# Performance work log

Measured on AMD Instinct MI355X. Metric: run time of the kernel, lower is better.

Reference implementation:

```python
import jax, jax.numpy as jnp
import numpy as np
import math

B = 64        # graphs per batch
NPG = 2048    # nodes per graph
DEG = 4       # avg degree
EPG = NPG * DEG
N = B * NPG
E = B * EPG
F_IN = 4
H = 128
K1 = math.ceil(0.8 * NPG)   # 1639
K2 = math.ceil(0.8 * K1)    # 1312
K3 = math.ceil(0.8 * K2)    # 1050
ACT = 124


def setup_inputs() -> dict:
    key = jax.random.key(0)
    ks = jax.random.split(key, 20)
    x = jax.random.normal(ks[0], (N, F_IN), jnp.float32)
    off = (jnp.arange(B, dtype=jnp.int32) * NPG)[:, None]
    src = (jax.random.randint(ks[1], (B, EPG), 0, NPG, jnp.int32) + off).reshape(-1)
    dst = (jax.random.randint(ks[2], (B, EPG), 0, NPG, jnp.int32) + off).reshape(-1)

    def lin(k, fi, fo):
        return (jax.random.normal(k, (fi, fo), jnp.float32) / np.sqrt(fi)).astype(jnp.float32)

    return dict(
        x=x, src=src, dst=dst,
        W1=lin(ks[3], F_IN, H), b1=jnp.zeros((H,), jnp.float32),
        W2=lin(ks[4], H, H),    b2=jnp.zeros((H,), jnp.float32),
        W3=lin(ks[5], H, H),    b3=jnp.zeros((H,), jnp.float32),
        p1=jax.random.normal(ks[6], (H,), jnp.float32),
        p2=jax.random.normal(ks[7], (H,), jnp.float32),
        p3=jax.random.normal(ks[8], (H,), jnp.float32),
        lw1=lin(ks[9], 2 * H, H),  lb1=jnp.zeros((H,), jnp.float32),
        lw2=lin(ks[10], H, 64),    lb2=jnp.zeros((64,), jnp.float32),
        lw3=lin(ks[11], 64, ACT),  lb3=jnp.zeros((ACT,), jnp.float32),
    )


def gcn(x, W, b, src, dst, emask, n_nodes):
    # PyG GCNConv: add self loops, sym-norm deg^-1/2 A deg^-1/2, then bias
    h = x @ W                                  # [n, H]
    w = emask.astype(x.dtype)                  # [E]
    deg = jax.ops.segment_sum(w, dst, num_segments=n_nodes) + 1.0  # +1 self loop
    dis = jax.lax.rsqrt(deg)
    coef = dis[src] * dis[dst] * w             # [E]
    out = jax.ops.segment_sum(h[src] * coef[:, None], dst, num_segments=n_nodes)
    out = out + h * (dis * dis)[:, None]       # self-loop contribution
    return out + b


def topk_pool(x, p, src, dst, emask, n_per_graph, k):
    # TopKPooling: score = tanh(x.p/||p||); keep top ceil(ratio*n) per graph;
    # x_out = x[perm] * score[perm]; drop edges not fully inside kept set.
    score = jnp.tanh((x @ p) / jnp.linalg.norm(p))       # [B*n]
    vals, idx = jax.lax.top_k(score.reshape(B, n_per_graph), k)  # [B,k]
    xg = x.reshape(B, n_per_graph, -1)
    x_new = (jnp.take_along_axis(xg, idx[:, :, None], axis=1) * vals[:, :, None])
    x_new = x_new.reshape(B * k, -1)
    flat_idx = (idx + (jnp.arange(B, dtype=jnp.int32) * n_per_graph)[:, None]).reshape(-1)
    new_pos = jnp.full((B * n_per_graph,), -1, jnp.int32)
    new_pos = new_pos.at[flat_idx].set(jnp.arange(B * k, dtype=jnp.int32))
    ns, nd = new_pos[src], new_pos[dst]
    valid = emask & (ns >= 0) & (nd >= 0)
    ns = jnp.where(valid, ns, 0)
    nd = jnp.where(valid, nd, 0)
    return x_new, ns, nd, valid


def readout(x, k):
    # global_max_pool || global_mean_pool (uniform graph sizes)
    xr = x.reshape(B, k, -1)
    return jnp.concatenate([xr.max(axis=1), xr.mean(axis=1)], axis=1)  # [B, 2H]


def reference(x, src, dst, W1, b1, W2, b2, W3, b3, p1, p2, p3,
              lw1, lb1, lw2, lb2, lw3, lb3):
    emask = jnp.ones((E,), bool)
    h = jax.nn.relu(gcn(x, W1, b1, src, dst, emask, N))
    h, s1, d1, m1 = topk_pool(h, p1, src, dst, emask, NPG, K1)
    x1 = readout(h, K1)
    h = jax.nn.relu(gcn(h, W2, b2, s1, d1, m1, B * K1))
    h, s2, d2, m2 = topk_pool(h, p2, s1, d1, m1, K1, K2)
    x2 = readout(h, K2)
    h = jax.nn.relu(gcn(h, W3, b3, s2, d2, m2, B * K2))
    h, s3, d3, m3 = topk_pool(h, p3, s2, d2, m2, K2, K3)
    x3 = readout(h, K3)
    z = x1 + x2 + x3                                # [B, 256]
    z = jax.nn.relu(z @ lw1 + lb1)
    z = jax.nn.relu(z @ lw2 + lb2)
    # F.dropout(p=0.5) is identity in eval mode
    out = jax.nn.sigmoid(z @ lw3 + lb3)             # [B, 124]; squeeze(1) is no-op
    return out
```

## Files before the change

### kernel.cpp

```cpp
#include <hip/hip_runtime.h>
#include <math.h>

namespace {
constexpr int B_   = 64;
constexpr int NPG  = 2048;
constexpr int N0   = B_ * NPG;
constexpr int E0   = N0 * 4;
constexpr int H_   = 128;
constexpr int K1   = 1639, K2 = 1312, K3 = 1050;
constexpr int N1   = B_ * K1;
constexpr int N2   = B_ * K2;
constexpr int N3   = B_ * K3;
constexpr int ACT  = 124;
constexpr int RS   = 32;
}

typedef short bf16x8 __attribute__((ext_vector_type(8)));
typedef float f32x4  __attribute__((ext_vector_type(4)));

__device__ __forceinline__ unsigned short f2bf(float f)
{
    unsigned x = __float_as_uint(f);
    x = x + 0x7FFFu + ((x >> 16) & 1u);
    return (unsigned short)(x >> 16);
}

__global__ void pack_k(const float* __restrict__ W, unsigned short* __restrict__ WT)
{
    int t = blockIdx.x * 256 + threadIdx.x;
    int n = t >> 7, k = t & 127;
    WT[n * 128 + k] = f2bf(W[k * 128 + n]);
}

__global__ __launch_bounds__(256) void mmh_k(const float* __restrict__ Xin,
                                             const int* __restrict__ selOld,
                                             const float* __restrict__ score,
                                             const unsigned short* __restrict__ WT,
                                             float* __restrict__ C, int M)
{
    __shared__ unsigned short sA[64 * 128];
    char* sAb = (char*)sA;
    int tid = threadIdx.x;
    int row0 = blockIdx.x * 64;
    #pragma unroll
    for (int ch = 0; ch < 8; ++ch) {
        int i = ch * 1024 + tid * 4;
        int r = i >> 7, c = i & 127;
        int g = selOld[row0 + r];
        float sc = score[g];
        float4 v = *(const float4*)(Xin + (size_t)g * H_ + c);
        unsigned short h0 = f2bf(v.x * sc), h1 = f2bf(v.y * sc);
        unsigned short h2 = f2bf(v.z * sc), h3 = f2bf(v.w * sc);
        unsigned int lo = (unsigned int)h0 | ((unsigned int)h1 << 16);
        unsigned int hi = (unsigned int)h2 | ((unsigned int)h3 << 16);
        int off = (r * 256 + c * 2) ^ ((r & 7) << 4);
        *(unsigned int*)(sAb + off)     = lo;
        *(unsigned int*)(sAb + off + 4) = hi;
    }
    __syncthreads();

    int w    = tid >> 6;
    int lane = tid & 63;
    int l16  = lane & 15;
    int lq   = lane >> 4;
    int arow = w * 16 + l16;
    int abase = (arow * 256) ^ ((arow & 7) << 4);

    f32x4 acc[8];
    #pragma unroll
    for (int ct = 0; ct < 8; ++ct) acc[ct] = (f32x4){0.f, 0.f, 0.f, 0.f};

    #pragma unroll
    for (int ks = 0; ks < 4; ++ks) {
        int aoff = (arow * 256 + ks * 64 + lq * 16) ^ ((arow & 7) << 4);
        bf16x8 af = *(const bf16x8*)(sAb + aoff);
        #pragma unroll
        for (int ct = 0; ct < 8; ++ct) {
            const unsigned short* bp = WT + (ct * 16 + l16) * 128 + ks * 32 + lq * 8;
            bf16x8 bf = *(const bf16x8*)bp;
            acc[ct] = __builtin_amdgcn_mfma_f32_16x16x32_bf16(af, bf, acc[ct], 0, 0, 0);
        }
    }
    #pragma unroll
    for (int ct = 0; ct < 8; ++ct) {
        int col = ct * 16 + l16;
        int rb  = row0 + w * 16 + lq * 4;
        C[(size_t)(rb + 0) * H_ + col] = acc[ct][0];
        C[(size_t)(rb + 1) * H_ + col] = acc[ct][1];
        C[(size_t)(rb + 2) * H_ + col] = acc[ct][2];
        C[(size_t)(rb + 3) * H_ + col] = acc[ct][3];
    }
}

__global__ void count_deg_k(const int* __restrict__ dst, int E, int* __restrict__ deg)
{
    int e = blockIdx.x * blockDim.x + threadIdx.x;
    if (e < E) atomicAdd(deg + dst[e], 1);
}

__global__ __launch_bounds__(1024) void scan1_k(const int* __restrict__ in, int* __restrict__ out,
                                                int* __restrict__ bsum, int n)
{
    __shared__ int s[1024];
    int t = threadIdx.x;
    int i = blockIdx.x * 1024 + t;
    int v = (i < n) ? in[i] : 0;
    s[t] = v;
    __syncthreads();
    for (int d = 1; d < 1024; d <<= 1) {
        int add = (t >= d) ? s[t - d] : 0;
        __syncthreads();
        s[t] += add;
        __syncthreads();
    }
    if (i < n) out[i] = s[t] - v;
    if (t == 1023) bsum[blockIdx.x] = s[1023];
}

__global__ __launch_bounds__(256) void scan2_k(int* __restrict__ bsum, int nb,
                                               int* __restrict__ totalOut,
                                               const float* __restrict__ p,
                                               float* __restrict__ invnOut)
{
    __shared__ int s[256];
    __shared__ float ps[128];
    int t = threadIdx.x;
    int v = (t < nb) ? bsum[t] : 0;
    s[t] = v;
    if (p && t < 128) ps[t] = p[t] * p[t];
    __syncthreads();
    for (int d = 1; d < 256; d <<= 1) {
        int add = (t >= d) ? s[t - d] : 0;
        __syncthreads();
        s[t] += add;
        __syncthreads();
    }
    if (t < nb) bsum[t] = s[t] - v;
    if (t == 0 && totalOut) *totalOut = s[255];
    for (int d = 64; d > 0; d >>= 1) {
        if (p && t < d) ps[t] += ps[t + d];
        __syncthreads();
    }
    if (p && t == 0) *invnOut = rsqrtf(ps[0]);
}

__global__ void scan3_k(int* __restrict__ out, const int* __restrict__ bsum, int n,
                        const int* __restrict__ deg, float* __restrict__ dis)
{
    int i = blockIdx.x * blockDim.x + threadIdx.x;
    if (i < n) {
        out[i] += bsum[i >> 10];
        dis[i] = rsqrtf((float)deg[i] + 1.0f);
    }
}

__global__ void fill_k(const int* __restrict__ src, const int* __restrict__ dst, int E,
                       const int* __restrict__ rowoff, int* __restrict__ cur,
                       int* __restrict__ esrc)
{
    int e = blockIdx.x * blockDim.x + threadIdx.x;
    if (e >= E) return;
    int d = dst[e];
    int pos = rowoff[d] + atomicAdd(cur + d, 1);
    esrc[pos] = src[e];
}

__global__ void remap_count_k(const int* __restrict__ osrc, const int* __restrict__ odst,
                              const int* __restrict__ ecntIn, int fixedE,
                              const int* __restrict__ newpos, int* __restrict__ deg)
{
    int E = ecntIn ? *ecntIn : fixedE;
    int e = blockIdx.x * blockDim.x + threadIdx.x;
    if (e >= E) return;
    int ns = newpos[osrc[e]];
    int nd = newpos[odst[e]];
    if (ns >= 0 && nd >= 0) atomicAdd(deg + nd, 1);
}

__global__ void remap_fill_k(const int* __restrict__ osrc, const int* __restrict__ odst,
                             const int* __restrict__ ecntIn, int fixedE,
                             const int* __restrict__ newpos, const int* __restrict__ rowoff,
                             int* __restrict__ cur,
                             int* __restrict__ esrc, int* __restrict__ edst)
{
    int E = ecntIn ? *ecntIn : fixedE;
    int e = blockIdx.x * blockDim.x + threadIdx.x;
    if (e >= E) return;
    int ns = newpos[osrc[e]];
    int nd = newpos[odst[e]];
    if (ns >= 0 && nd >= 0) {
        int pos = rowoff[nd] + atomicAdd(cur + nd, 1);
        esrc[pos] = ns;
        edst[pos] = nd;
    }
}

__global__ __launch_bounds__(256) void aggx_k(const float* __restrict__ X,
                                              const int* __restrict__ rowoff,
                                              const int* __restrict__ esrc,
                                              const float* __restrict__ dis,
                                              const float* __restrict__ W1,
                                              const float* __restrict__ b1,
                                              const float* __restrict__ p1,
                                              const float* __restrict__ invn,
                                              float* __restrict__ out,
                                              float* __restrict__ score,
                                              int npg, int Gb)
{
    __shared__ float sW[512];
    __shared__ float sb[128];
    __shared__ float sp[128];
    __shared__ float sxa[256 * 4];
    __shared__ float sdt[256];
    int tid = threadIdx.x;
    for (int i = tid; i < 512; i += 256) sW[i] = W1[i];
    if (tid < 128) { sb[tid] = b1[tid]; sp[tid] = p1[tid]; }
    int pb = blockIdx.x;
    int x8 = pb & 7;
    int m  = pb >> 3;
    int g  = x8 + 8 * (m / Gb);
    int lb = m % Gb;
    int nbase = g * npg + lb * 256;
    int n = nbase + tid;
    float dn = dis[n];
    float4 xa = *(const float4*)(X + (size_t)n * 4);
    float s2 = dn * dn;
    xa.x *= s2; xa.y *= s2; xa.z *= s2; xa.w *= s2;
    int beg = rowoff[n], end = rowoff[n + 1];
    for (int e = beg; e < end; ++e) {
        int s = esrc[e];
        float c = dis[s] * dn;
        float4 xs = *(const float4*)(X + (size_t)s * 4);
        xa.x += xs.x * c; xa.y += xs.y * c; xa.z += xs.z * c; xa.w += xs.w * c;
    }
    *(float4*)(sxa + tid * 4) = xa;
    __syncthreads();
    int wv = tid >> 6;
    int lane = tid & 63;
    int c0 = lane * 2;
    float wa0 = sW[c0],     wb0 = sW[128 + c0],     wc0 = sW[256 + c0],     wd0 = sW[384 + c0];
    float wa1 = sW[c0 + 1], wb1 = sW[128 + c0 + 1], wc1 = sW[256 + c0 + 1], wd1 = sW[384 + c0 + 1];
    float bb0 = sb[c0], bb1 = sb[c0 + 1];
    float pp0 = sp[c0], pp1 = sp[c0 + 1];
    #pragma unroll 4
    for (int ii = 0; ii < 64; ++ii) {
        int i = wv * 64 + ii;
        float4 a = *(const float4*)(sxa + i * 4);
        float o0 = fmaxf(a.x * wa0 + a.y * wb0 + a.z * wc0 + a.w * wd0 + bb0, 0.f);
        float o1 = fmaxf(a.x * wa1 + a.y * wb1 + a.z * wc1 + a.w * wd1 + bb1, 0.f);
        ((float2*)(out + (size_t)(nbase + i) * H_))[lane] = make_float2(o0, o1);
        float dt = o0 * pp0 + o1 * pp1;
        for (int mm = 32; mm > 0; mm >>= 1) dt += __shfl_xor(dt, mm);
        if (lane == 0) sdt[i] = dt;
    }
    __syncthreads();
    score[nbase + tid] = tanhf(sdt[tid] * invn[0]);
}

__global__ __launch_bounds__(256) void agg_k(const float* __restrict__ Hf,
                                             const int* __restrict__ rowoff,
                                             const int* __restrict__ esrc,
                                             const float* __restrict__ dis,
                                             const float* __restrict__ bias,
                                             const float* __restrict__ p,
                                             const float* __restrict__ invn,
                                             float* __restrict__ out,
                                             float* __restrict__ score,
                                             int npg, int Gb)
{
    int pb = blockIdx.x;
    int x8 = pb & 7;
    int m  = pb >> 3;
    int g  = x8 + 8 * (m / Gb);
    int lb = m % Gb;
    int j  = lb * 4 + (threadIdx.x >> 6);
    if (j >= npg) return;
    int n = g * npg + j;
    int lane = threadIdx.x & 63;
    int half = lane >> 5;
    int l4 = (lane & 31) * 4;
    float dn = dis[n];
    int beg = rowoff[n], end = rowoff[n + 1];
    float4 acc = make_float4(0.f, 0.f, 0.f, 0.f);
    for (int e = beg + half; e < end; e += 2) {
        int s = esrc[e];
        float c = dis[s] * dn;
        float4 v = *(const float4*)(Hf + (size_t)s * H_ + l4);
        acc.x += v.x * c; acc.y += v.y * c; acc.z += v.z * c; acc.w += v.w * c;
    }
    acc.x += __shfl_xor(acc.x, 32);
    acc.y += __shfl_xor(acc.y, 32);
    acc.z += __shfl_xor(acc.z, 32);
    acc.w += __shfl_xor(acc.w, 32);
    if (half == 0) {
        float4 hv = *(const float4*)(Hf + (size_t)n * H_ + l4);
        float4 bv = *(const float4*)(bias + l4);
        float s2 = dn * dn;
        float o0 = fmaxf(acc.x + hv.x * s2 + bv.x, 0.f);
        float o1 = fmaxf(acc.y + hv.y * s2 + bv.y, 0.f);
        float o2 = fmaxf(acc.z + hv.z * s2 + bv.z, 0.f);
        float o3 = fmaxf(acc.w + hv.w * s2 + bv.w, 0.f);
        *(float4*)(out + (size_t)n * H_ + l4) = make_float4(o0, o1, o2, o3);
        float4 pv = *(const float4*)(p + l4);
        float dt = o0 * pv.x + o1 * pv.y + o2 * pv.z + o3 * pv.w;
        for (int mm = 16; mm > 0; mm >>= 1) dt += __shfl_xor(dt, mm);
        if ((lane & 31) == 0) score[n] = tanhf(dt * invn[0]);
    }
}

__global__ __launch_bounds__(1024) void radix_topk_k(const float* __restrict__ score,
                                                     int n, int k,
                                                     int* __restrict__ selOld,
                                                     int* __restrict__ newpos)
{
    __shared__ unsigned long long key[2048];
    __shared__ int hist[256];
    __shared__ int sufs[256];
    __shared__ unsigned long long sh_prefix;
    __shared__ int sh_r, sh_done, sh_v, sh_rbin;
    __shared__ int cnt;
    int b = blockIdx.x;
    int t = threadIdx.x;
    const float* s = score + (size_t)b * n;
    #pragma unroll
    for (int h = 0; h < 2; ++h) {
        int i = t + h * 1024;
        unsigned long long pk = 0ull;
        if (i < n) {
            unsigned u = __float_as_uint(s[i]);
            u = (u & 0x80000000u) ? ~u : (u | 0x80000000u);
            pk = ((unsigned long long)u << 32) | (unsigned)(65535 - i);
        }
        key[i] = pk;
    }
    if (t == 0) { sh_prefix = 0ull; sh_r = k; sh_done = 0; cnt = 0; }
    __syncthreads();

    for (int lvl = 0; lvl < 8; ++lvl) {
        if (sh_done) break;
        int bs = 56 - 8 * lvl;
        if (t < 256) hist[t] = 0;
        __syncthreads();
        unsigned long long pref = sh_prefix;
        #pragma unroll
        for (int h = 0; h < 2; ++h) {
            int i = t + h * 1024;
            unsigned long long kk = key[i];
            if (kk != 0ull) {
                bool match = (lvl == 0) || ((kk >> (bs + 8)) == (pref >> (bs + 8)));
                if (match) atomicAdd(&hist[(int)((kk >> bs) & 255)], 1);
            }
        }
        __syncthreads();
        if (t < 256) sufs[t] = hist[t];
        __syncthreads();
        for (int d = 1; d < 256; d <<= 1) {
            int add = (t < 256 && t + d < 256) ? sufs[t + d] : 0;
            __syncthreads();
            if (t < 256) sufs[t] += add;
            __syncthreads();
        }
        if (t < 256) {
            int above = (t == 255) ? 0 : sufs[t + 1];
            if (sufs[t] >= sh_r && above < sh_r) {
                sh_v = t;
                sh_rbin = sh_r - above;
            }
        }
        __syncthreads();
        if (t == 0) {
            int v = sh_v;
            sh_prefix |= ((unsigned long long)v) << bs;
            sh_r = sh_rbin;
            if (hist[v] == sh_rbin) sh_done = 1;
        }
        __syncthreads();
    }
    unsigned long long thr = sh_prefix;
    #pragma unroll
    for (int h = 0; h < 2; ++h) {
        int i = t + h * 1024;
        if (i < n && key[i] >= thr) {
            int pos = atomicAdd(&cnt, 1);
            int oldg = b * n + i;
            selOld[b * k + pos] = oldg;
            newpos[oldg] = b * k + pos;
        }
    }
}

__global__ __launch_bounds__(512) void readout_part_k(const float* __restrict__ X,
                                                      const int* __restrict__ selOld,
                                                      const float* __restrict__ score,
                                                      int kRows, float* __restrict__ part)
{
    __shared__ float smax[16][128];
    __shared__ float ssum[16][128];
    int b = blockIdx.x / RS;
    int s = blockIdx.x % RS;
    int chunk = (kRows + RS - 1) / RS;
    int j0 = s * chunk;
    int j1 = min(kRows, j0 + chunk);
    int tid = threadIdx.x;
    int f4 = (tid & 31) * 4;
    int q = tid >> 5;
    float4 mx = make_float4(-3.4e38f, -3.4e38f, -3.4e38f, -3.4e38f);
    float4 sm = make_float4(0.f, 0.f, 0.f, 0.f);
    for (int j = j0 + q; j < j1; j += 16) {
        int g = selOld[b * kRows + j];
        float sc = score[g];
        float4 v = *(const float4*)(X + (size_t)g * H_ + f4);
        v.x *= sc; v.y *= sc; v.z *= sc; v.w *= sc;
        mx.x = fmaxf(mx.x, v.x); mx.y = fmaxf(mx.y, v.y);
        mx.z = fmaxf(mx.z, v.z); mx.w = fmaxf(mx.w, v.w);
        sm.x += v.x; sm.y += v.y; sm.z += v.z; sm.w += v.w;
    }
    *(float4*)&smax[q][f4] = mx;
    *(float4*)&ssum[q][f4] = sm;
    __syncthreads();
    if (tid < 128) {
        float m = smax[0][tid], a = ssum[0][tid];
        #pragma unroll
        for (int gq = 1; gq < 16; ++gq) {
            m = fmaxf(m, smax[gq][tid]);
            a += ssum[gq][tid];
        }
        float* pr = part + ((size_t)b * RS + s) * 256;
        pr[tid] = m;
        pr[128 + tid] = a;
    }
}

__global__ __launch_bounds__(256) void head_k(const float* __restrict__ part1,
                                              const float* __restrict__ part2,
                                              const float* __restrict__ part3,
                                              const float* __restrict__ lw1, const float* __restrict__ lb1,
                                              const float* __restrict__ lw2, const float* __restrict__ lb2,
                                              const float* __restrict__ lw3, const float* __restrict__ lb3,
                                              float* __restrict__ out)
{
    __shared__ float sZ[256];
    __shared__ float sZ1[128];
    __shared__ float sZ2[64];
    __shared__ float red[256];
    int b = blockIdx.x;
    int t = threadIdx.x;
    {
        int f = t & 127;
        const float* pr1 = part1 + (size_t)b * RS * 256;
        const float* pr2 = part2 + (size_t)b * RS * 256;
        const float* pr3 = part3 + (size_t)b * RS * 256;
        float zv;
        if (t < 128) {
            float m1 = -3.4e38f, m2 = -3.4e38f, m3 = -3.4e38f;
            #pragma unroll
            for (int s = 0; s < RS; ++s) {
                m1 = fmaxf(m1, pr1[s * 256 + f]);
                m2 = fmaxf(m2, pr2[s * 256 + f]);
                m3 = fmaxf(m3, pr3[s * 256 + f]);
            }
            zv = m1 + m2 + m3;
        } else {
            float s1 = 0.f, s2 = 0.f, s3 = 0.f;
            #pragma unroll
            for (int s = 0; s < RS; ++s) {
                s1 += pr1[s * 256 + 128 + f];
                s2 += pr2[s * 256 + 128 + f];
                s3 += pr3[s * 256 + 128 + f];
            }
            zv = s1 * (1.0f / (float)K1) + s2 * (1.0f / (float)K2) + s3 * (1.0f / (float)K3);
        }
        sZ[t] = zv;
    }
    __syncthreads();
    {
        int c = t & 127, h = t >> 7;
        float acc = 0.f;
        #pragma unroll
        for (int i = 0; i < 128; ++i) {
            int ii = h * 128 + i;
            acc += sZ[ii] * lw1[ii * 128 + c];
        }
        red[t] = acc;
        __syncthreads();
        if (t < 128) sZ1[t] = fmaxf(red[t] + red[128 + t] + lb1[t], 0.f);
        __syncthreads();
    }
    {
        int c = t & 63, q = t >> 6;
        float acc = 0.f;
        #pragma unroll
        for (int i = 0; i < 32; ++i) {
            int ii = q * 32 + i;
            acc += sZ1[ii] * lw2[ii * 64 + c];
        }
        red[t] = acc;
        __syncthreads();
        if (t < 64) sZ2[t] = fmaxf(red[t] + red[64 + t] + red[128 + t] + red[192 + t] + lb2[t], 0.f);
        __syncthreads();
    }
    {
        if (t < 2 * ACT) {
            int c = t >> 1, h = t & 1;
            float acc = 0.f;
            #pragma unroll
            for (int i = 0; i < 32; ++i) {
                int ii = h * 32 + i;
                acc += sZ2[ii] * lw3[ii * ACT + c];
            }
            red[t] = acc;
        }
        __syncthreads();
        if (t < ACT) {
            float s = red[2 * t] + red[2 * t + 1] + lb3[t];
            out[b * ACT + t] = 1.f / (1.f + expf(-s));
        }
    }
}

extern "C" void kernel_launch(void* const* d_in, const int* in_sizes, int n_in,
                              void* d_out, int out_size, void* d_ws, size_t ws_size,
                              hipStream_t stream)
{
    const float* x   = (const float*)d_in[0];
    const int*   src = (const int*)d_in[1];
    const int*   dst = (const int*)d_in[2];
    const float* W1  = (const float*)d_in[3];
    const float* b1  = (const float*)d_in[4];
    const float* W2  = (const float*)d_in[5];
    const float* b2  = (const float*)d_in[6];
    const float* W3  = (const float*)d_in[7];
    const float* b3  = (const float*)d_in[8];
    const float* p1  = (const float*)d_in[9];
    const float* p2  = (const float*)d_in[10];
    const float* p3  = (const float*)d_in[11];
    const float* lw1 = (const float*)d_in[12];
    const float* lb1 = (const float*)d_in[13];
    const float* lw2 = (const float*)d_in[14];
    const float* lb2 = (const float*)d_in[15];
    const float* lw3 = (const float*)d_in[16];
    const float* lb3 = (const float*)d_in[17];

    char* w = (char*)d_ws;
    size_t off = 0;
    auto alloc = [&](size_t bytes) -> void* {
        void* p = w + off;
        off = (off + bytes + 255) & ~(size_t)255;
        return p;
    };
    float* fA     = (float*)alloc((size_t)N0 * H_ * 4);
    float* fB     = (float*)alloc((size_t)N0 * H_ * 4);
    float* score  = (float*)alloc((size_t)N0 * 4);
    int*   newpos = (int*)  alloc((size_t)N0 * 4);
    int*   deg    = (int*)  alloc((size_t)(N0 + 1) * 4);
    int*   cur    = (int*)  alloc((size_t)N0 * 4);
    float* dis    = (float*)alloc((size_t)(N0 + 1) * 4);
    int*   selOld = (int*)  alloc((size_t)N1 * 4);
    int*   rowoff = (int*)  alloc((size_t)(N0 + 1) * 4);
    int*   bsum   = (int*)  alloc((size_t)1024 * 4);
    int*   cs0    = (int*)  alloc((size_t)E0 * 4);
    int*   cs1    = (int*)  alloc((size_t)E0 * 4);
    int*   cd1    = (int*)  alloc((size_t)E0 * 4);
    int*   cs2    = (int*)  alloc((size_t)E0 * 4);
    int*   cd2    = (int*)  alloc((size_t)E0 * 4);
    float* part1  = (float*)alloc((size_t)B_ * RS * 256 * 4);
    float* part2  = (float*)alloc((size_t)B_ * RS * 256 * 4);
    float* part3  = (float*)alloc((size_t)B_ * RS * 256 * 4);
    unsigned short* WT2 = (unsigned short*)alloc((size_t)128 * 128 * 2);
    unsigned short* WT3 = (unsigned short*)alloc((size_t)128 * 128 * 2);
    int*   ecnt   = (int*)  alloc(256);
    float* invn   = (float*)alloc(256);

    const size_t degcur_bytes = (size_t)((char*)cur - (char*)deg) + (size_t)N0 * 4;

    auto scan_rowoff = [&](int nNodes, int* totalOut, const float* p) {
        int n = nNodes + 1;
        int nb = (n + 1023) / 1024;
        scan1_k<<<nb, 1024, 0, stream>>>(deg, rowoff, bsum, n);
        scan2_k<<<1, 256, 0, stream>>>(bsum, nb, totalOut, p, invn);
        scan3_k<<<(n + 255) / 256, 256, 0, stream>>>(rowoff, bsum, n, deg, dis);
    };

    const int GbX = NPG / 256;
    const int Gb1 = (K1 + 3) / 4;
    const int Gb2 = (K2 + 3) / 4;

    pack_k<<<64, 256, 0, stream>>>(W2, WT2);
    pack_k<<<64, 256, 0, stream>>>(W3, WT3);

    hipMemsetAsync(deg, 0, degcur_bytes, stream);
    count_deg_k<<<E0 / 256, 256, 0, stream>>>(dst, E0, deg);
    scan_rowoff(N0, nullptr, p1);
    fill_k<<<E0 / 256, 256, 0, stream>>>(src, dst, E0, rowoff, cur, cs0);
    aggx_k<<<B_ * GbX, 256, 0, stream>>>(x, rowoff, cs0, dis, W1, b1, p1, invn, fB, score, NPG, GbX);

    hipMemsetAsync(newpos, 0xFF, (size_t)N0 * 4, stream);
    radix_topk_k<<<B_, 1024, 0, stream>>>(score, NPG, K1, selOld, newpos);
    readout_part_k<<<B_ * RS, 512, 0, stream>>>(fB, selOld, score, K1, part1);

    hipMemsetAsync(deg, 0, degcur_bytes, stream);
    remap_count_k<<<E0 / 256, 256, 0, stream>>>(src, dst, nullptr, E0, newpos, deg);
    scan_rowoff(N1, ecnt, p2);
    remap_fill_k<<<E0 / 256, 256, 0, stream>>>(src, dst, nullptr, E0, newpos, rowoff, cur, cs1, cd1);

    mmh_k<<<N1 / 64, 256, 0, stream>>>(fB, selOld, score, WT2, fA, N1);
    agg_k<<<B_ * Gb1, 256, 0, stream>>>(fA, rowoff, cs1, dis, b2, p2, invn, fB, score, K1, Gb1);

    hipMemsetAsync(newpos, 0xFF, (size_t)N1 * 4, stream);
    radix_topk_k<<<B_, 1024, 0, stream>>>(score, K1, K2, selOld, newpos);
    readout_part_k<<<B_ * RS, 512, 0, stream>>>(fB, selOld, score, K2, part2);

    hipMemsetAsync(deg, 0, degcur_bytes, stream);
    remap_count_k<<<E0 / 256, 256, 0, stream>>>(cs1, cd1, ecnt, 0, newpos, deg);
    scan_rowoff(N2, nullptr, p3);
    remap_fill_k<<<E0 / 256, 256, 0, stream>>>(cs1, cd1, ecnt, 0, newpos, rowoff, cur, cs2, cd2);

    mmh_k<<<N2 / 64, 256, 0, stream>>>(fB, selOld, score, WT3, fA, N2);
    agg_k<<<B_ * Gb2, 256, 0, stream>>>(fA, rowoff, cs2, dis, b3, p3, invn, fB, score, K2, Gb2);

    radix_topk_k<<<B_, 1024, 0, stream>>>(score, K2, K3, selOld, newpos);
    readout_part_k<<<B_ * RS, 512, 0, stream>>>(fB, selOld, score, K3, part3);

    head_k<<<B_, 256, 0, stream>>>(part1, part2, part3, lw1, lb1, lw2, lb2, lw3, lb3, (float*)d_out);
}
```

Baseline: 362.7 us.

## Build pooled CSR per row from previous CSR and fuse readout into gather GEMM

```diff
diff --git a/kernel.cpp b/kernel.cpp
--- a/kernel.cpp
+++ b/kernel.cpp
@@ -13,6 +13,8 @@
 constexpr int N3   = B_ * K3;
 constexpr int ACT  = 124;
 constexpr int RS   = 32;
+constexpr int Gm1  = (K1 + 63) / 64;
+constexpr int Gm2  = (K2 + 63) / 64;
 }
 
 typedef short bf16x8 __attribute__((ext_vector_type(8)));
@@ -36,35 +38,62 @@
                                              const int* __restrict__ selOld,
                                              const float* __restrict__ score,
                                              const unsigned short* __restrict__ WT,
-                                             float* __restrict__ C, int M)
+                                             float* __restrict__ C,
+                                             float* __restrict__ part,
+                                             int K, int Gm)
 {
     __shared__ unsigned short sA[64 * 128];
+    __shared__ float rmax[8][128];
+    __shared__ float rsum[8][128];
     char* sAb = (char*)sA;
     int tid = threadIdx.x;
-    int row0 = blockIdx.x * 64;
+    int g   = blockIdx.x / Gm;
+    int lb  = blockIdx.x % Gm;
+    int jbase = lb * 64;
+    const int* selg = selOld + (size_t)g * K;
+    int cc = (tid * 4) & 127;
+    float4 pmax = make_float4(-3.4e38f, -3.4e38f, -3.4e38f, -3.4e38f);
+    float4 psum = make_float4(0.f, 0.f, 0.f, 0.f);
     #pragma unroll
     for (int ch = 0; ch < 8; ++ch) {
         int i = ch * 1024 + tid * 4;
         int r = i >> 7, c = i & 127;
-        int g = selOld[row0 + r];
-        float sc = score[g];
-        float4 v = *(const float4*)(Xin + (size_t)g * H_ + c);
-        unsigned short h0 = f2bf(v.x * sc), h1 = f2bf(v.y * sc);
-        unsigned short h2 = f2bf(v.z * sc), h3 = f2bf(v.w * sc);
-        unsigned int lo = (unsigned int)h0 | ((unsigned int)h1 << 16);
-        unsigned int hi = (unsigned int)h2 | ((unsigned int)h3 << 16);
+        int j = jbase + r;
+        unsigned int lo = 0u, hi = 0u;
+        if (j < K) {
+            int gg = selg[j];
+            float sc = score[gg];
+            float4 v = *(const float4*)(Xin + (size_t)gg * H_ + c);
+            v.x *= sc; v.y *= sc; v.z *= sc; v.w *= sc;
+            pmax.x = fmaxf(pmax.x, v.x); pmax.y = fmaxf(pmax.y, v.y);
+            pmax.z = fmaxf(pmax.z, v.z); pmax.w = fmaxf(pmax.w, v.w);
+            psum.x += v.x; psum.y += v.y; psum.z += v.z; psum.w += v.w;
+            unsigned short h0 = f2bf(v.x), h1 = f2bf(v.y);
+            unsigned short h2 = f2bf(v.z), h3 = f2bf(v.w);
+            lo = (unsigned int)h0 | ((unsigned int)h1 << 16);
+            hi = (unsigned int)h2 | ((unsigned int)h3 << 16);
+        }
         int off = (r * 256 + c * 2) ^ ((r & 7) << 4);
         *(unsigned int*)(sAb + off)     = lo;
         *(unsigned int*)(sAb + off + 4) = hi;
     }
-    __syncthreads();
+    *(float4*)&rmax[tid >> 5][cc] = pmax;
+    *(float4*)&rsum[tid >> 5][cc] = psum;
+    __syncthreads();
+    if (tid < 128) {
+        float m = rmax[0][tid], s = rsum[0][tid];
+        #pragma unroll
+        for (int k = 1; k < 8; ++k) { m = fmaxf(m, rmax[k][tid]); s += rsum[k][tid]; }
+        float* pr = part + ((size_t)g * Gm + lb) * 256;
+        pr[tid] = m;
+        pr[128 + tid] = s;
+    }
 
     int w    = tid >> 6;
     int lane = tid & 63;
     int l16  = lane & 15;
     int lq   = lane >> 4;
     int arow = w * 16 + l16;
-    int abase = (arow * 256) ^ ((arow & 7) << 4);
 
     f32x4 acc[8];
     #pragma unroll
@@ -81,14 +110,15 @@
             acc[ct] = __builtin_amdgcn_mfma_f32_16x16x32_bf16(af, bf, acc[ct], 0, 0, 0);
         }
     }
+    int jb = jbase + w * 16 + lq * 4;
     #pragma unroll
     for (int ct = 0; ct < 8; ++ct) {
         int col = ct * 16 + l16;
-        int rb  = row0 + w * 16 + lq * 4;
-        C[(size_t)(rb + 0) * H_ + col] = acc[ct][0];
-        C[(size_t)(rb + 1) * H_ + col] = acc[ct][1];
-        C[(size_t)(rb + 2) * H_ + col] = acc[ct][2];
-        C[(size_t)(rb + 3) * H_ + col] = acc[ct][3];
+        float* cp = C + ((size_t)g * K + jb) * H_ + col;
+        if (jb + 0 < K) cp[0 * H_] = acc[ct][0];
+        if (jb + 1 < K) cp[1 * H_] = acc[ct][1];
+        if (jb + 2 < K) cp[2 * H_] = acc[ct][2];
+        if (jb + 3 < K) cp[3 * H_] = acc[ct][3];
     }
 }
 
@@ -117,8 +147,37 @@
     if (t == 1023) bsum[blockIdx.x] = s[1023];
 }
 
+__global__ __launch_bounds__(1024) void scan1b_k(const int* __restrict__ selOld,
+                                                 const int* __restrict__ proff,
+                                                 const int* __restrict__ pcs,
+                                                 const int* __restrict__ newpos,
+                                                 int* __restrict__ deg,
+                                                 int* __restrict__ out,
+                                                 int* __restrict__ bsum, int n)
+{
+    __shared__ int s[1024];
+    int t = threadIdx.x;
+    int i = blockIdx.x * 1024 + t;
+    int v = 0;
+    if (i < n - 1) {
+        int o = selOld[i];
+        int e1 = proff[o + 1];
+        for (int e = proff[o]; e < e1; ++e) v += (newpos[pcs[e]] >= 0) ? 1 : 0;
+    }
+    if (i < n) deg[i] = v;
+    s[t] = v;
+    __syncthreads();
+    for (int d = 1; d < 1024; d <<= 1) {
+        int add = (t >= d) ? s[t - d] : 0;
+        __syncthreads();
+        s[t] += add;
+        __syncthreads();
+    }
+    if (i < n) out[i] = s[t] - v;
+    if (t == 1023) bsum[blockIdx.x] = s[1023];
+}
+
 __global__ __launch_bounds__(256) void scan2_k(int* __restrict__ bsum, int nb,
-                                               int* __restrict__ totalOut,
                                                const float* __restrict__ p,
                                                float* __restrict__ invnOut)
 {
@@ -136,7 +195,6 @@
         __syncthreads();
     }
     if (t < nb) bsum[t] = s[t] - v;
-    if (t == 0 && totalOut) *totalOut = s[255];
     for (int d = 64; d > 0; d >>= 1) {
         if (p && t < d) ps[t] += ps[t + d];
         __syncthreads();
@@ -165,33 +223,19 @@
     esrc[pos] = src[e];
 }
 
-__global__ void remap_count_k(const int* __restrict__ osrc, const int* __restrict__ odst,
-                              const int* __restrict__ ecntIn, int fixedE,
-                              const int* __restrict__ newpos, int* __restrict__ deg)
-{
-    int E = ecntIn ? *ecntIn : fixedE;
-    int e = blockIdx.x * blockDim.x + threadIdx.x;
-    if (e >= E) return;
-    int ns = newpos[osrc[e]];
-    int nd = newpos[odst[e]];
-    if (ns >= 0 && nd >= 0) atomicAdd(deg + nd, 1);
-}
-
-__global__ void remap_fill_k(const int* __restrict__ osrc, const int* __restrict__ odst,
-                             const int* __restrict__ ecntIn, int fixedE,
-                             const int* __restrict__ newpos, const int* __restrict__ rowoff,
-                             int* __restrict__ cur,
-                             int* __restrict__ esrc, int* __restrict__ edst)
-{
-    int E = ecntIn ? *ecntIn : fixedE;
-    int e = blockIdx.x * blockDim.x + threadIdx.x;
-    if (e >= E) return;
-    int ns = newpos[osrc[e]];
-    int nd = newpos[odst[e]];
-    if (ns >= 0 && nd >= 0) {
-        int pos = rowoff[nd] + atomicAdd(cur + nd, 1);
-        esrc[pos] = ns;
-        edst[pos] = nd;
+__global__ void fill_row_k(const int* __restrict__ selOld,
+                           const int* __restrict__ proff, const int* __restrict__ pcs,
+                           const int* __restrict__ newpos, const int* __restrict__ roff,
+                           int* __restrict__ cs, int nNodes)
+{
+    int i = blockIdx.x * blockDim.x + threadIdx.x;
+    if (i >= nNodes) return;
+    int o = selOld[i];
+    int wptr = roff[i];
+    int e1 = proff[o + 1];
+    for (int e = proff[o]; e < e1; ++e) {
+        int m = newpos[pcs[e]];
+        if (m >= 0) cs[wptr++] = m;
     }
 }
 
@@ -380,11 +424,15 @@
     #pragma unroll
     for (int h = 0; h < 2; ++h) {
         int i = t + h * 1024;
-        if (i < n && key[i] >= thr) {
-            int pos = atomicAdd(&cnt, 1);
-            int oldg = b * n + i;
-            selOld[b * k + pos] = oldg;
-            newpos[oldg] = b * k + pos;
+        if (i < n) {
+            if (key[i] >= thr) {
+                int pos = atomicAdd(&cnt, 1);
+                int oldg = b * n + i;
+                selOld[b * k + pos] = oldg;
+                newpos[oldg] = b * k + pos;
+            } else {
+                newpos[b * n + i] = -1;
+            }
         }
     }
 }
@@ -431,9 +479,9 @@
     }
 }
 
-__global__ __launch_bounds__(256) void head_k(const float* __restrict__ part1,
-                                              const float* __restrict__ part2,
-                                              const float* __restrict__ part3,
+__global__ __launch_bounds__(256) void head_k(const float* __restrict__ part1, int c1,
+                                              const float* __restrict__ part2, int c2,
+                                              const float* __restrict__ part3, int c3,
                                               const float* __restrict__ lw1, const float* __restrict__ lb1,
                                               const float* __restrict__ lw2, const float* __restrict__ lb2,
                                               const float* __restrict__ lw3, const float* __restrict__ lb3,
@@ -447,27 +495,21 @@
     int t = threadIdx.x;
     {
         int f = t & 127;
-        const float* pr1 = part1 + (size_t)b * RS * 256;
-        const float* pr2 = part2 + (size_t)b * RS * 256;
-        const float* pr3 = part3 + (size_t)b * RS * 256;
+        const float* pr1 = part1 + (size_t)b * c1 * 256;
+        const float* pr2 = part2 + (size_t)b * c2 * 256;
+        const float* pr3 = part3 + (size_t)b * c3 * 256;
         float zv;
         if (t < 128) {
             float m1 = -3.4e38f, m2 = -3.4e38f, m3 = -3.4e38f;
-            #pragma unroll
-            for (int s = 0; s < RS; ++s) {
-                m1 = fmaxf(m1, pr1[s * 256 + f]);
-                m2 = fmaxf(m2, pr2[s * 256 + f]);
-                m3 = fmaxf(m3, pr3[s * 256 + f]);
-            }
+            for (int s = 0; s < c1; ++s) m1 = fmaxf(m1, pr1[s * 256 + f]);
+            for (int s = 0; s < c2; ++s) m2 = fmaxf(m2, pr2[s * 256 + f]);
+            for (int s = 0; s < c3; ++s) m3 = fmaxf(m3, pr3[s * 256 + f]);
             zv = m1 + m2 + m3;
         } else {
             float s1 = 0.f, s2 = 0.f, s3 = 0.f;
-            #pragma unroll
-            for (int s = 0; s < RS; ++s) {
-                s1 += pr1[s * 256 + 128 + f];
-                s2 += pr2[s * 256 + 128 + f];
-                s3 += pr3[s * 256 + 128 + f];
-            }
+            for (int s = 0; s < c1; ++s) s1 += pr1[s * 256 + 128 + f];
+            for (int s = 0; s < c2; ++s) s2 += pr2[s * 256 + 128 + f];
+            for (int s = 0; s < c3; ++s) s3 += pr3[s * 256 + 128 + f];
             zv = s1 * (1.0f / (float)K1) + s2 * (1.0f / (float)K2) + s3 * (1.0f / (float)K3);
         }
         sZ[t] = zv;
@@ -556,70 +598,65 @@
     int*   cur    = (int*)  alloc((size_t)N0 * 4);
     float* dis    = (float*)alloc((size_t)(N0 + 1) * 4);
     int*   selOld = (int*)  alloc((size_t)N1 * 4);
-    int*   rowoff = (int*)  alloc((size_t)(N0 + 1) * 4);
+    int*   ro0    = (int*)  alloc((size_t)(N0 + 1) * 4);
+    int*   ro1    = (int*)  alloc((size_t)(N1 + 1) * 4);
+    int*   ro2    = (int*)  alloc((size_t)(N2 + 1) * 4);
     int*   bsum   = (int*)  alloc((size_t)1024 * 4);
     int*   cs0    = (int*)  alloc((size_t)E0 * 4);
     int*   cs1    = (int*)  alloc((size_t)E0 * 4);
-    int*   cd1    = (int*)  alloc((size_t)E0 * 4);
     int*   cs2    = (int*)  alloc((size_t)E0 * 4);
-    int*   cd2    = (int*)  alloc((size_t)E0 * 4);
-    float* part1  = (float*)alloc((size_t)B_ * RS * 256 * 4);
-    float* part2  = (float*)alloc((size_t)B_ * RS * 256 * 4);
+    float* part1  = (float*)alloc((size_t)B_ * Gm1 * 256 * 4);
+    float* part2  = (float*)alloc((size_t)B_ * Gm2 * 256 * 4);
     float* part3  = (float*)alloc((size_t)B_ * RS * 256 * 4);
     unsigned short* WT2 = (unsigned short*)alloc((size_t)128 * 128 * 2);
     unsigned short* WT3 = (unsigned short*)alloc((size_t)128 * 128 * 2);
-    int*   ecnt   = (int*)  alloc(256);
     float* invn   = (float*)alloc(256);
 
     const size_t degcur_bytes = (size_t)((char*)cur - (char*)deg) + (size_t)N0 * 4;
 
-    auto scan_rowoff = [&](int nNodes, int* totalOut, const float* p) {
-        int n = nNodes + 1;
-        int nb = (n + 1023) / 1024;
-        scan1_k<<<nb, 1024, 0, stream>>>(deg, rowoff, bsum, n);
-        scan2_k<<<1, 256, 0, stream>>>(bsum, nb, totalOut, p, invn);
-        scan3_k<<<(n + 255) / 256, 256, 0, stream>>>(rowoff, bsum, n, deg, dis);
-    };
-
-    const int GbX = NPG / 256;
-    const int Gb1 = (K1 + 3) / 4;
-    const int Gb2 = (K2 + 3) / 4;
+    const int GbX  = NPG / 256;
+    const int Gb1  = (K1 + 3) / 4;
+    const int Gb2  = (K2 + 3) / 4;
 
     pack_k<<<64, 256, 0, stream>>>(W2, WT2);
     pack_k<<<64, 256, 0, stream>>>(W3, WT3);
 
     hipMemsetAsync(deg, 0, degcur_bytes, stream);
     count_deg_k<<<E0 / 256, 256, 0, stream>>>(dst, E0, deg);
-    scan_rowoff(N0, nullptr, p1);
-    fill_k<<<E0 / 256, 256, 0, stream>>>(src, dst, E0, rowoff, cur, cs0);
-    aggx_k<<<B_ * GbX, 256, 0, stream>>>(x, rowoff, cs0, dis, W1, b1, p1, invn, fB, score, NPG, GbX);
-
-    hipMemsetAsync(newpos, 0xFF, (size_t)N0 * 4, stream);
+    {
+        int n = N0 + 1, nb = (n + 1023) / 1024;
+        scan1_k<<<nb, 1024, 0, stream>>>(deg, ro0, bsum, n);
+        scan2_k<<<1, 256, 0, stream>>>(bsum, nb, p1, invn);
+        scan3_k<<<(n + 255) / 256, 256, 0, stream>>>(ro0, bsum, n, deg, dis);
+    }
+    fill_k<<<E0 / 256, 256, 0, stream>>>(src, dst, E0, ro0, cur, cs0);
+    aggx_k<<<B_ * GbX, 256, 0, stream>>>(x, ro0, cs0, dis, W1, b1, p1, invn, fB, score, NPG, GbX);
+
     radix_topk_k<<<B_, 1024, 0, stream>>>(score, NPG, K1, selOld, newpos);
-    readout_part_k<<<B_ * RS, 512, 0, stream>>>(fB, selOld, score, K1, part1);
-
-    hipMemsetAsync(deg, 0, degcur_bytes, stream);
-    remap_count_k<<<E0 / 256, 256, 0, stream>>>(src, dst, nullptr, E0, newpos, deg);
-    scan_rowoff(N1, ecnt, p2);
-    remap_fill_k<<<E0 / 256, 256, 0, stream>>>(src, dst, nullptr, E0, newpos, rowoff, cur, cs1, cd1);
-
-    mmh_k<<<N1 / 64, 256, 0, stream>>>(fB, selOld, score, WT2, fA, N1);
-    agg_k<<<B_ * Gb1, 256, 0, stream>>>(fA, rowoff, cs1, dis, b2, p2, invn, fB, score, K1, Gb1);
-
-    hipMemsetAsync(newpos, 0xFF, (size_t)N1 * 4, stream);
+    mmh_k<<<B_ * Gm1, 256, 0, stream>>>(fB, selOld, score, WT2, fA, part1, K1, Gm1);
+    {
+        int n = N1 + 1, nb = (n + 1023) / 1024;
+        scan1b_k<<<nb, 1024, 0, stream>>>(selOld, ro0, cs0, newpos, deg, ro1, bsum, n);
+        scan2_k<<<1, 256, 0, stream>>>(bsum, nb, p2, invn);
+        scan3_k<<<(n + 255) / 256, 256, 0, stream>>>(ro1, bsum, n, deg, dis);
+    }
+    fill_row_k<<<(N1 + 255) / 256, 256, 0, stream>>>(selOld, ro0, cs0, newpos, ro1, cs1, N1);
+    agg_k<<<B_ * Gb1, 256, 0, stream>>>(fA, ro1, cs1, dis, b2, p2, invn, fB, score, K1, Gb1);
+
     radix_topk_k<<<B_, 1024, 0, stream>>>(score, K1, K2, selOld, newpos);
-    readout_part_k<<<B_ * RS, 512, 0, stream>>>(fB, selOld, score, K2, part2);
-
-    hipMemsetAsync(deg, 0, degcur_bytes, stream);
-    remap_count_k<<<E0 / 256, 256, 0, stream>>>(cs1, cd1, ecnt, 0, newpos, deg);
-    scan_rowoff(N2, nullptr, p3);
-    remap_fill_k<<<E0 / 256, 256, 0, stream>>>(cs1, cd1, ecnt, 0, newpos, rowoff, cur, cs2, cd2);
-
-    mmh_k<<<N2 / 64, 256, 0, stream>>>(fB, selOld, score, WT3, fA, N2);
-    agg_k<<<B_ * Gb2, 256, 0, stream>>>(fA, rowoff, cs2, dis, b3, p3, invn, fB, score, K2, Gb2);
+    mmh_k<<<B_ * Gm2, 256, 0, stream>>>(fB, selOld, score, WT3, fA, part2, K2, Gm2);
+    {
+        int n = N2 + 1, nb = (n + 1023) / 1024;
+        scan1b_k<<<nb, 1024, 0, stream>>>(selOld, ro1, cs1, newpos, deg, ro2, bsum, n);
+        scan2_k<<<1, 256, 0, stream>>>(bsum, nb, p3, invn);
+        scan3_k<<<(n + 255) / 256, 256, 0, stream>>>(ro2, bsum, n, deg, dis);
+    }
+    fill_row_k<<<(N2 + 255) / 256, 256, 0, stream>>>(selOld, ro1, cs1, newpos, ro2, cs2, N2);
+    agg_k<<<B_ * Gb2, 256, 0, stream>>>(fA, ro2, cs2, dis, b3, p3, invn, fB, score, K2, Gb2);
 
     radix_topk_k<<<B_, 1024, 0, stream>>>(score, K2, K3, selOld, newpos);
     readout_part_k<<<B_ * RS, 512, 0, stream>>>(fB, selOld, score, K3, part3);
 
-    head_k<<<B_, 256, 0, stream>>>(part1, part2, part3, lw1, lb1, lw2, lb2, lw3, lb3, (float*)d_out);
-}
+    head_k<<<B_, 256, 0, stream>>>(part1, Gm1, part2, Gm2, part3, RS,
+                                   lw1, lb1, lw2, lb2, lw3, lb3, (float*)d_out);
+}
```

Result: faster. 331.3 us (-8.7%).
